# Kernel tuning notes

Measured on AMD Instinct MI355X. Metric: run time of the kernel, lower is better.

## Reference

```python
import jax, jax.numpy as jnp
import numpy as np

N_CHANNELS = 512
D_K = 64
N_HEADS = N_CHANNELS // D_K  # 8
SCALE = 1.0 / np.sqrt(np.sqrt(D_K))
EPS = 1e-8


def pixnorm(x, axis=-1):
    return x * jax.lax.rsqrt(jnp.mean(x * x, axis=axis, keepdims=True) + EPS)


def setup_inputs() -> dict:
    key = jax.random.key(0)
    k1, k2, k3 = jax.random.split(key, 3)
    x = jax.random.normal(k1, (16, N_CHANNELS, 32, 32), dtype=jnp.float32)
    # 1x1 conv weights (bias=False) stored as [out, in]
    w_proj = jax.random.normal(k2, (3 * N_CHANNELS, N_CHANNELS), dtype=jnp.float32) * (1.0 / np.sqrt(N_CHANNELS))
    w_out = jax.random.normal(k3, (N_CHANNELS, N_CHANNELS), dtype=jnp.float32) * (1.0 / np.sqrt(N_CHANNELS))
    return {"x": x, "w_proj": w_proj, "w_out": w_out}


def reference(x, w_proj, w_out):
    B, C, H, W = x.shape
    S = H * W
    # tokens: [B, S, C]
    xt = x.reshape(B, C, S).transpose(0, 2, 1)
    # 1x1 conv projection -> [B, S, 3C]
    h = jnp.einsum('bsc,oc->bso', xt, w_proj)
    qkv = h.reshape(B, S, N_HEADS, 3 * D_K)
    q, k, v = jnp.split(qkv, 3, axis=-1)  # each [B, S, H, d]
    q = pixnorm(q)
    k = pixnorm(k)
    v = pixnorm(v)
    attn = jnp.einsum('bihd,bjhd->bijh', q * SCALE, k * SCALE)
    attn = jax.nn.softmax(attn, axis=2)
    res = jnp.einsum('bijh,bjhd->bihd', attn, v)  # [B, S, H, d]
    res = res.reshape(B, S, C)
    res = jnp.einsum('bsc,oc->bso', res, w_out)
    res = res.transpose(0, 2, 1).reshape(B, C, H, W)
    return x + res
```

## Files before the change

### kernel.cpp

```cpp
#include <hip/hip_runtime.h>
#include <hip/hip_bf16.h>
#include <math.h>

typedef float f32x4 __attribute__((ext_vector_type(4)));
typedef __bf16 bf16x8 __attribute__((ext_vector_type(8)));
typedef __bf16 bf16x4 __attribute__((ext_vector_type(4)));
typedef unsigned u32x4 __attribute__((ext_vector_type(4)));

#define DEVFN static __device__ __forceinline__

DEVFN void gload16(const void* g, void* l) {
  __builtin_amdgcn_global_load_lds(
      (const __attribute__((address_space(1))) unsigned int*)g,
      (__attribute__((address_space(3))) unsigned int*)l, 16, 0, 0);
}

DEVFN f32x4 mfma16(bf16x8 a, bf16x8 b, f32x4 c) {
  return __builtin_amdgcn_mfma_f32_16x16x32_bf16(a, b, c, 0, 0, 0);
}

DEVFN unsigned cvtpk(float lo, float hi) {
  unsigned r;
  asm("v_cvt_pk_bf16_f32 %0, %1, %2" : "=v"(r) : "v"(lo), "v"(hi));
  return r;
}

#define WAITV4() asm volatile("s_waitcnt vmcnt(4)" ::: "memory")
#define WAITV0() asm volatile("s_waitcnt vmcnt(0)" ::: "memory")

__global__ __launch_bounds__(256) void cast_weights_k(
    const float* __restrict__ wp, const float* __restrict__ wo,
    __bf16* __restrict__ wpb, __bf16* __restrict__ wob) {
  int i = blockIdx.x * 256 + threadIdx.x;
  if (i < 1536 * 512) {
    wpb[i] = (__bf16)wp[i];
  } else {
    int j = i - 1536 * 512;
    wob[j] = (__bf16)wo[j];
  }
}

__global__ __launch_bounds__(256) void transpose_x_k(const float* __restrict__ x,
                                                     __bf16* __restrict__ xt) {
  __shared__ float tile[64][65];
  int b = blockIdx.z, c0 = blockIdx.y * 64, s0 = blockIdx.x * 64;
  int t = threadIdx.x;
  int r = t >> 2, q = (t & 3) << 4;
  const float* src = x + ((size_t)(b * 512 + c0 + r)) * 1024 + s0 + q;
#pragma unroll
  for (int i = 0; i < 4; i++) {
    float4 f = *reinterpret_cast<const float4*>(src + i * 4);
    tile[r][q + i * 4 + 0] = f.x;
    tile[r][q + i * 4 + 1] = f.y;
    tile[r][q + i * 4 + 2] = f.z;
    tile[r][q + i * 4 + 3] = f.w;
  }
  __syncthreads();
  bf16x8 o0, o1;
#pragma unroll
  for (int i = 0; i < 8; i++) o0[i] = (__bf16)tile[q + i][r];
#pragma unroll
  for (int i = 0; i < 8; i++) o1[i] = (__bf16)tile[q + 8 + i][r];
  __bf16* dst = xt + ((size_t)(b * 1024 + s0 + r)) * 512 + c0 + q;
  *reinterpret_cast<bf16x8*>(dst) = o0;
  *reinterpret_cast<bf16x8*>(dst + 8) = o1;
}

template <int MODE>
__global__ __launch_bounds__(256) void gemm_bt_k(
    const __bf16* __restrict__ A, const __bf16* __restrict__ Bt,
    float* __restrict__ Cf, const float* __restrict__ Xres,
    __bf16* __restrict__ Qo, __bf16* __restrict__ Ko, __bf16* __restrict__ Vto) {
  __shared__ __attribute__((aligned(16))) char smem[32768];
  const int K = 512;
  int p = blockIdx.x, xcd = p & 7, idx = p >> 3;
  int m0, n0, z;
  if (MODE == 2) {
    m0 = (xcd * 16 + idx / 12) * 128;
    n0 = (idx % 12) * 128;
    z = 0;
  } else {
    z = xcd * 2 + idx / 32;
    int rem = idx % 32;
    m0 = (rem >> 3) * 128;
    n0 = (rem & 7) * 128;
    Bt += (size_t)z * (1024L * 512);
  }
  int tid = threadIdx.x, wave = tid >> 6, lane = tid & 63;
  int fr = lane & 15, fq = lane >> 4;
  int wm = (wave >> 1) * 64, wn = (wave & 1) * 64;
  f32x4 acc[4][4] = {};
  int offs[2], rr[2], scc[2];
#pragma unroll
  for (int i = 0; i < 2; i++) {
    offs[i] = wave * 2048 + i * 1024 + lane * 16;
    rr[i] = offs[i] >> 6;
    scc[i] = (offs[i] & 63) ^ (((rr[i] ^ (rr[i] >> 2)) & 3) << 4);
  }
  int rdsw = (fr ^ (fr >> 2)) & 3;
  const char* Ap = (const char*)A;
  const char* Bp = (const char*)Bt;

#define GSTAGE(k0_, buf_)                                                       \
  {                                                                             \
    char* as_ = smem + (buf_)*8192;                                             \
    char* bs_ = smem + 16384 + (buf_)*8192;                                     \
    _Pragma("unroll") for (int i = 0; i < 2; i++)                               \
        gload16(Ap + (size_t)(m0 + rr[i]) * 1024 + (k0_)*2 + scc[i],            \
                as_ + offs[i]);                                                 \
    _Pragma("unroll") for (int i = 0; i < 2; i++)                               \
        gload16(Bp + (size_t)(n0 + rr[i]) * 1024 + (k0_)*2 + scc[i],            \
                bs_ + offs[i]);                                                 \
  }

  GSTAGE(0, 0);
  GSTAGE(32, 1);
  int cur = 0;
  for (int k0 = 0; k0 < K; k0 += 32) {
    if (k0 + 32 < K) WAITV4(); else WAITV0();
    __builtin_amdgcn_s_barrier();
    __builtin_amdgcn_sched_barrier(0);
    const char* as = smem + cur * 8192;
    const char* bs = smem + 16384 + cur * 8192;
    bf16x8 af[4], bfr[4];
#pragma unroll
    for (int mi = 0; mi < 4; mi++)
      af[mi] = *reinterpret_cast<const bf16x8*>(
          as + (wm + mi * 16 + fr) * 64 + ((fq ^ rdsw) << 4));
#pragma unroll
    for (int ni = 0; ni < 4; ni++)
      bfr[ni] = *reinterpret_cast<const bf16x8*>(
          bs + (wn + ni * 16 + fr) * 64 + ((fq ^ rdsw) << 4));
    __builtin_amdgcn_s_setprio(1);
#pragma unroll
    for (int mi = 0; mi < 4; mi++)
#pragma unroll
      for (int ni = 0; ni < 4; ni++)
        acc[mi][ni] = mfma16(af[mi], bfr[ni], acc[mi][ni]);
    __builtin_amdgcn_s_setprio(0);
    __builtin_amdgcn_s_barrier();
    if (k0 + 64 < K) GSTAGE(k0 + 64, cur);
    cur ^= 1;
  }
#undef GSTAGE

  if (MODE == 1) {
    float* Co = Cf + (size_t)z * (512L * 1024);
    const float* Xr = Xres + (size_t)z * (512L * 1024);
#pragma unroll
    for (int mi = 0; mi < 4; mi++)
#pragma unroll
      for (int i = 0; i < 4; i++) {
        int row = m0 + wm + mi * 16 + fq * 4 + i;
#pragma unroll
        for (int ni = 0; ni < 4; ni++) {
          size_t idxo = (size_t)row * 1024 + n0 + wn + ni * 16 + fr;
          Co[idxo] = acc[mi][ni][i] + Xr[idxo];
        }
      }
  } else {
    int g0 = n0 + wn;
    int head = g0 / 192;
    int grp = (g0 >> 6) % 3;
    int b = m0 >> 10, sb = m0 & 1023;
    int bh = b * 8 + head;
    float nrm[4][4];
#pragma unroll
    for (int mi = 0; mi < 4; mi++)
#pragma unroll
      for (int i = 0; i < 4; i++) {
        float ss = 0.f;
#pragma unroll
        for (int ni = 0; ni < 4; ni++) ss += acc[mi][ni][i] * acc[mi][ni][i];
#pragma unroll
        for (int off = 1; off < 16; off <<= 1) ss += __shfl_xor(ss, off);
        float nv = rsqrtf(ss * (1.0f / 64.0f) + 1e-8f);
        if (grp == 0) nv *= 0.18033688011112042f;
        nrm[mi][i] = nv;
      }
    if (grp < 2) {
      __bf16* dst = (grp == 0 ? Qo : Ko) + (size_t)bh * 65536;
#pragma unroll
      for (int mi = 0; mi < 4; mi++)
#pragma unroll
        for (int i = 0; i < 4; i++) {
          int s = sb + wm + mi * 16 + fq * 4 + i;
#pragma unroll
          for (int ni = 0; ni < 4; ni++)
            dst[(size_t)s * 64 + ni * 16 + fr] = (__bf16)(acc[mi][ni][i] * nrm[mi][i]);
        }
    }
    __syncthreads();
    if (grp == 2) {
#pragma unroll
      for (int mi = 0; mi < 4; mi++)
#pragma unroll
        for (int i = 0; i < 4; i++) {
          int r = wm + mi * 16 + fq * 4 + i;
#pragma unroll
          for (int ni = 0; ni < 4; ni++) {
            int col2 = (2 * (ni * 16 + fr)) ^ ((r & 31) << 2);
            *(__bf16*)(smem + r * 128 + col2) = (__bf16)(acc[mi][ni][i] * nrm[mi][i]);
          }
        }
    }
    __syncthreads();
    if (grp == 2) {
      int sl = wm + lane;
      int l = sl & 63;
      int pl = ((l >> 2) & 3) * 16 + (l >> 4) * 4 + (l & 3);
      __bf16* vdst = Vto + (size_t)bh * 65536 + sb + (sl & 64) + pl;
#pragma unroll 8
      for (int d = 0; d < 64; d++) {
        __bf16 v = *(const __bf16*)(smem + sl * 128 + ((2 * d) ^ ((sl & 31) << 2)));
        vdst[(size_t)d * 1024] = v;
      }
    }
  }
}

__global__ __launch_bounds__(256, 4) void attn_k(const __bf16* __restrict__ Q,
                                                 const __bf16* __restrict__ Kb,
                                                 const __bf16* __restrict__ Vt,
                                                 __bf16* __restrict__ Res) {
  __shared__ __attribute__((aligned(16))) char lds[32768];
  int p = blockIdx.x;
  int v = (p & 7) * 128 + (p >> 3);
  int qt = v & 7, bh = v >> 3;
  int wave = threadIdx.x >> 6, lane = threadIdx.x & 63;
  int fr = lane & 15, fq = lane >> 4;
  const __bf16* Qb = Q + (size_t)bh * 65536;
  const char* Kbase = (const char*)(Kb + (size_t)bh * 65536);
  const char* Vbase = (const char*)(Vt + (size_t)bh * 65536);
  bf16x8 qf[2][2];
#pragma unroll
  for (int qs = 0; qs < 2; qs++)
#pragma unroll
    for (int kk = 0; kk < 2; kk++)
      qf[qs][kk] = *reinterpret_cast<const bf16x8*>(
          Qb + (size_t)(qt * 128 + qs * 64 + wave * 16 + fr) * 64 + kk * 32 + fq * 8);

  bf16x8 ones;
#pragma unroll
  for (int j = 0; j < 8; j++) ones[j] = (__bf16)1.0f;

  f32x4 oa[2][4] = {};
  f32x4 lacc[2] = {};

  int o0 = wave * 2048 + lane * 16;
  int o1 = o0 + 1024;
  int r0 = o0 >> 7, c0 = o0 & 127, r1 = o1 >> 7, c1 = o1 & 127;
  int s0 = c0 ^ ((r0 & 7) << 4), s1 = c1 ^ ((r1 & 7) << 4);
  int swr = (fr & 7) << 4;

#define STAGE(kt_, buf_)                                                        \
  {                                                                             \
    char* ks_ = lds + (buf_)*8192;                                              \
    char* vs_ = lds + 16384 + (buf_)*8192;                                      \
    gload16(Kbase + (size_t)(kt_)*8192 + r0 * 128 + s0, ks_ + o0);              \
    gload16(Kbase + (size_t)(kt_)*8192 + r1 * 128 + s1, ks_ + o1);              \
    gload16(Vbase + (size_t)r0 * 2048 + (kt_)*128 + s0, vs_ + o0);              \
    gload16(Vbase + (size_t)r1 * 2048 + (kt_)*128 + s1, vs_ + o1);              \
  }

  STAGE(0, 0);
  STAGE(1, 1);
  for (int kt = 0; kt < 16; kt++) {
    int cur = kt & 1;
    if (kt < 15) WAITV4(); else WAITV0();
    __builtin_amdgcn_s_barrier();
    __builtin_amdgcn_sched_barrier(0);
    const char* ksc = lds + cur * 8192;
    const char* vsc = lds + 16384 + cur * 8192;
    f32x4 sa[2][4] = {};
    __builtin_amdgcn_s_setprio(1);
#pragma unroll
    for (int ni = 0; ni < 4; ni++) {
      bf16x8 kf0 = *reinterpret_cast<const bf16x8*>(
          ksc + (ni * 16 + fr) * 128 + ((fq * 16) ^ swr));
      bf16x8 kf1 = *reinterpret_cast<const bf16x8*>(
          ksc + (ni * 16 + fr) * 128 + ((64 + fq * 16) ^ swr));
#pragma unroll
      for (int qs = 0; qs < 2; qs++) {
        sa[qs][ni] = mfma16(kf0, qf[qs][0], sa[qs][ni]);
        sa[qs][ni] = mfma16(kf1, qf[qs][1], sa[qs][ni]);
      }
    }
    __builtin_amdgcn_s_setprio(0);
    bf16x8 pb[2][2];
#pragma unroll
    for (int qs = 0; qs < 2; qs++) {
#pragma unroll
      for (int ni = 0; ni < 4; ni++)
#pragma unroll
        for (int i = 0; i < 4; i++)
          sa[qs][ni][i] = __builtin_amdgcn_exp2f(sa[qs][ni][i]);
#pragma unroll
      for (int kk2 = 0; kk2 < 2; kk2++) {
        u32x4 u;
        u[0] = cvtpk(sa[qs][2 * kk2][0], sa[qs][2 * kk2][1]);
        u[1] = cvtpk(sa[qs][2 * kk2][2], sa[qs][2 * kk2][3]);
        u[2] = cvtpk(sa[qs][2 * kk2 + 1][0], sa[qs][2 * kk2 + 1][1]);
        u[3] = cvtpk(sa[qs][2 * kk2 + 1][2], sa[qs][2 * kk2 + 1][3]);
        pb[qs][kk2] = __builtin_bit_cast(bf16x8, u);
      }
      lacc[qs] = mfma16(ones, pb[qs][0], lacc[qs]);
      lacc[qs] = mfma16(ones, pb[qs][1], lacc[qs]);
    }
    __builtin_amdgcn_s_setprio(1);
#pragma unroll
    for (int nd = 0; nd < 4; nd++) {
      int vrow = (nd * 16 + fr) * 128;
#pragma unroll
      for (int kk2 = 0; kk2 < 2; kk2++) {
        bf16x8 vf = *reinterpret_cast<const bf16x8*>(
            vsc + vrow + ((fq * 32 + kk2 * 16) ^ swr));
#pragma unroll
        for (int qs = 0; qs < 2; qs++)
          oa[qs][nd] = mfma16(vf, pb[qs][kk2], oa[qs][nd]);
      }
    }
    __builtin_amdgcn_s_setprio(0);
    __builtin_amdgcn_s_barrier();
    if (kt + 2 < 16) STAGE(kt + 2, cur);
  }
  int b = bh >> 3, hd = bh & 7;
#pragma unroll
  for (int qs = 0; qs < 2; qs++) {
    int q = qt * 128 + qs * 64 + wave * 16 + fr;
    float inv_l = 1.0f / lacc[qs][0];
    __bf16* dst = Res + ((size_t)(b * 1024 + q)) * 512 + hd * 64 + fq * 4;
#pragma unroll
    for (int nd = 0; nd < 4; nd++) {
      bf16x4 ov;
#pragma unroll
      for (int i = 0; i < 4; i++) ov[i] = (__bf16)(oa[qs][nd][i] * inv_l);
      *reinterpret_cast<bf16x4*>(dst + nd * 16) = ov;
    }
  }
#undef STAGE
}

extern "C" void kernel_launch(void* const* d_in, const int* in_sizes, int n_in,
                              void* d_out, int out_size, void* d_ws, size_t ws_size,
                              hipStream_t stream) {
  const float* x = (const float*)d_in[0];
  const float* wp = (const float*)d_in[1];
  const float* wo = (const float*)d_in[2];
  float* out = (float*)d_out;
  char* w = (char*)d_ws;
  __bf16* wpb = (__bf16*)(w);
  __bf16* wob = (__bf16*)(w + 1572864);
  __bf16* xt = (__bf16*)(w + 2097152);
  __bf16* Qb = (__bf16*)(w + 18874368);
  __bf16* Kb = (__bf16*)(w + 35651584);
  __bf16* Vtb = (__bf16*)(w + 52428800);
  __bf16* resb = (__bf16*)(w + 69206016);

  cast_weights_k<<<4096, 256, 0, stream>>>(wp, wo, wpb, wob);
  transpose_x_k<<<dim3(16, 8, 16), 256, 0, stream>>>(x, xt);
  gemm_bt_k<2><<<1536, 256, 0, stream>>>(xt, wpb, nullptr, nullptr, Qb, Kb, Vtb);
  attn_k<<<1024, 256, 0, stream>>>(Qb, Kb, Vtb, resb);
  gemm_bt_k<1><<<512, 256, 0, stream>>>(wob, resb, out, x, nullptr, nullptr,
                                        nullptr);
}
```

Before: 126.9 us.

## Rotate attention loop to compute next-tile QK^T at iteration end; cap GEMM occupancy

The attention main loop is rotated so that the QK^T MFMAs for tile kt+1 are issued at the end of iteration kt, right after staging tile kt+2 and waiting on its loads. The first tile's QK^T is peeled before the loop, and the last iteration breaks early. The intent is to give the scheduler a longer window between the softmax/PV phase and the next score computation, so load waits and barriers overlap better with MFMA work. Separately, the GEMM kernel gets a minimum-occupancy launch bound of 4 blocks, which can force register limits and risks spills.

```diff
diff --git a/kernel.cpp b/kernel.cpp
--- a/kernel.cpp
+++ b/kernel.cpp
@@ -67,7 +67,7 @@
 }
 
 template <int MODE>
-__global__ __launch_bounds__(256) void gemm_bt_k(
+__global__ __launch_bounds__(256, 4) void gemm_bt_k(
     const __bf16* __restrict__ A, const __bf16* __restrict__ Bt,
     float* __restrict__ Cf, const float* __restrict__ Xres,
     __bf16* __restrict__ Qo, __bf16* __restrict__ Ko, __bf16* __restrict__ Vto) {
@@ -263,30 +263,33 @@
     gload16(Vbase + (size_t)r1 * 2048 + (kt_)*128 + s1, vs_ + o1);              \
   }
 
+#define QKT(buf_)                                                               \
+  {                                                                             \
+    const char* ksc_ = lds + (buf_)*8192;                                       \
+    __builtin_amdgcn_s_setprio(1);                                              \
+    _Pragma("unroll") for (int ni = 0; ni < 4; ni++) {                          \
+      bf16x8 kf0 = *reinterpret_cast<const bf16x8*>(                            \
+          ksc_ + (ni * 16 + fr) * 128 + ((fq * 16) ^ swr));                     \
+      bf16x8 kf1 = *reinterpret_cast<const bf16x8*>(                            \
+          ksc_ + (ni * 16 + fr) * 128 + ((64 + fq * 16) ^ swr));                \
+      _Pragma("unroll") for (int qs = 0; qs < 2; qs++) {                        \
+        sa[qs][ni] = mfma16(kf0, qf[qs][0], sa[qs][ni]);                        \
+        sa[qs][ni] = mfma16(kf1, qf[qs][1], sa[qs][ni]);                        \
+      }                                                                         \
+    }                                                                           \
+    __builtin_amdgcn_s_setprio(0);                                              \
+  }
+
   STAGE(0, 0);
   STAGE(1, 1);
+  WAITV4();
+  __builtin_amdgcn_s_barrier();
+  __builtin_amdgcn_sched_barrier(0);
+  f32x4 sa[2][4] = {};
+  QKT(0);
   for (int kt = 0; kt < 16; kt++) {
     int cur = kt & 1;
-    if (kt < 15) WAITV4(); else WAITV0();
-    __builtin_amdgcn_s_barrier();
-    __builtin_amdgcn_sched_barrier(0);
-    const char* ksc = lds + cur * 8192;
     const char* vsc = lds + 16384 + cur * 8192;
-    f32x4 sa[2][4] = {};
-    __builtin_amdgcn_s_setprio(1);
-#pragma unroll
-    for (int ni = 0; ni < 4; ni++) {
-      bf16x8 kf0 = *reinterpret_cast<const bf16x8*>(
-          ksc + (ni * 16 + fr) * 128 + ((fq * 16) ^ swr));
-      bf16x8 kf1 = *reinterpret_cast<const bf16x8*>(
-          ksc + (ni * 16 + fr) * 128 + ((64 + fq * 16) ^ swr));
-#pragma unroll
-      for (int qs = 0; qs < 2; qs++) {
-        sa[qs][ni] = mfma16(kf0, qf[qs][0], sa[qs][ni]);
-        sa[qs][ni] = mfma16(kf1, qf[qs][1], sa[qs][ni]);
-      }
-    }
-    __builtin_amdgcn_s_setprio(0);
     bf16x8 pb[2][2];
 #pragma unroll
     for (int qs = 0; qs < 2; qs++) {
@@ -321,8 +324,21 @@
       }
     }
     __builtin_amdgcn_s_setprio(0);
+    if (kt == 15) break;
     __builtin_amdgcn_s_barrier();
-    if (kt + 2 < 16) STAGE(kt + 2, cur);
+    if (kt + 2 < 16) {
+      STAGE(kt + 2, cur);
+      WAITV4();
+    } else {
+      WAITV0();
+    }
+    __builtin_amdgcn_s_barrier();
+    __builtin_amdgcn_sched_barrier(0);
+#pragma unroll
+    for (int qs = 0; qs < 2; qs++)
+#pragma unroll
+      for (int ni = 0; ni < 4; ni++) sa[qs][ni] = (f32x4){0.f, 0.f, 0.f, 0.f};
+    QKT(cur ^ 1);
   }
   int b = bh >> 3, hd = bh & 7;
 #pragma unroll
@@ -339,6 +355,7 @@
     }
   }
 #undef STAGE
+#undef QKT
 }
 
 extern "C" void kernel_launch(void* const* d_in, const int* in_sizes, int n_in,
```

New measurement: 118.7 us. 6.4% less time.
